# Performance work log

Measured on AMD Instinct MI355X. Metric: run time of the kernel, lower is better.

The kernel has to match this reference:

```python
import jax, jax.numpy as jnp
import numpy as np

B, T, K = 32, 64, 5
VOCAB, DE, DA, DI, H = 32000, 300, 300, 2048, 512


def setup_inputs() -> dict:
    key = jax.random.key(0)
    ks = jax.random.split(key, 8)
    return {
        'top_k_attributes': jax.random.randint(ks[0], (B, K), 0, 1000, dtype=jnp.int32),
        'mean_image_features': jax.random.normal(ks[1], (B, DI), jnp.float32),
        'seq_inputs': jax.random.randint(ks[2], (B, T), 0, VOCAB, dtype=jnp.int32),
        'lengths': jax.random.randint(ks[3], (B,), 1, T + 1, dtype=jnp.int32),
        'word_emb': jax.random.normal(ks[4], (VOCAB, DE), jnp.float32) * 0.02,
        'attr_emb': jax.random.normal(ks[5], (1000, DA), jnp.float32) * 0.02,
        'lstm_kernel': jax.random.normal(ks[6], (DE + DI + DA + H, 4 * H), jnp.float32) * 0.02,
        'lstm_bias': jnp.zeros((4 * H,), jnp.float32),
        'W_logits': jax.random.normal(ks[7], (H, VOCAB), jnp.float32) * 0.02,
        'b_logits': jnp.zeros((VOCAB,), jnp.float32),
    }


def reference(top_k_attributes, mean_image_features, seq_inputs, lengths,
              word_emb, attr_emb, lstm_kernel, lstm_bias, W_logits, b_logits):
    # attribute features: lookup + mean over the K attributes
    attr_feats = attr_emb[top_k_attributes]              # [B,K,DA]
    mean_attr = attr_feats.mean(axis=1)                  # [B,DA]
    feats = jnp.concatenate([mean_image_features, mean_attr], axis=-1)  # [B,DI+DA]

    x = word_emb[seq_inputs]                             # [B,T,DE]
    # per-step cell input = concat(word_emb_t, image+attr features)
    inp = jnp.concatenate([x, jnp.broadcast_to(feats[:, None, :], (B, T, feats.shape[-1]))], axis=-1)

    def step(carry, x_t):
        h, c = carry
        z = jnp.concatenate([x_t, h], axis=-1) @ lstm_kernel + lstm_bias  # [B,4H]
        i, f, g, o = jnp.split(z, 4, axis=-1)
        c = jax.nn.sigmoid(f) * c + jax.nn.sigmoid(i) * jnp.tanh(g)
        h = jax.nn.sigmoid(o) * jnp.tanh(c)
        return (h, c), h

    h0 = jnp.zeros((B, H), inp.dtype)
    (_, _), h_seq = jax.lax.scan(step, (h0, h0), jnp.transpose(inp, (1, 0, 2)))
    h_seq = jnp.transpose(h_seq, (1, 0, 2))              # [B,T,H]

    # dynamic_rnn zeros activations past each sequence length
    mask = (jnp.arange(T)[None, :] < lengths[:, None])[:, :, None]
    h_seq = jnp.where(mask, h_seq, 0.0)

    logits = jnp.einsum('bth,hv->btv', h_seq, W_logits) + b_logits  # [B,T,V]
    return logits, jnp.argmax(logits, axis=-1).astype(jnp.int32)
```

## Files before the change

### kernel.cpp

```cpp
#include <hip/hip_runtime.h>
#include <hip/hip_bf16.h>
#include <math.h>

#define BATCH 32
#define TSEQ  64
#define KATTR 5
#define VOCAB 32000
#define DE    300
#define DA    300
#define DI    2048
#define HDIM  512
#define G4    2048
#define WOFF  (DE + DI + DA)

__global__ void zero_kernel(float* __restrict__ p, int n) {
    int i = blockIdx.x * blockDim.x + threadIdx.x;
    if (i < n) p[i] = 0.f;
}

__global__ void mean_attr_kernel(const int* __restrict__ topk,
                                 const float* __restrict__ attr_emb,
                                 float* __restrict__ mean_attr) {
    int b = blockIdx.x;
    int tid = threadIdx.x;
    if (tid < DA) {
        float s = 0.f;
        #pragma unroll
        for (int q = 0; q < KATTR; ++q) {
            int a = topk[b * KATTR + q];
            s += attr_emb[(size_t)a * DA + tid];
        }
        mean_attr[b * DA + tid] = s / (float)KATTR;
    }
}

__launch_bounds__(256)
__global__ void zf_kernel(const float* __restrict__ img,
                          const float* __restrict__ mean_attr,
                          const float* __restrict__ Wk,
                          const float* __restrict__ bias,
                          float* __restrict__ zf) {
    int b = blockIdx.y;
    int j = blockIdx.x * 256 + threadIdx.x;
    float acc = bias[j];
    const float* wimg = Wk + (size_t)DE * G4 + j;
    const float* irow = img + b * DI;
    #pragma unroll 8
    for (int k = 0; k < DI; ++k) acc += irow[k] * wimg[(size_t)k * G4];
    const float* wattr = Wk + (size_t)(DE + DI) * G4 + j;
    const float* arow = mean_attr + b * DA;
    #pragma unroll 4
    for (int k = 0; k < DA; ++k) acc += arow[k] * wattr[(size_t)k * G4];
    zf[b * G4 + j] = acc;
}

__launch_bounds__(256)
__global__ void whr_kernel(const float* __restrict__ Wk, float* __restrict__ Whr) {
    const int bid = blockIdx.x;
    const int tid = threadIdx.x;
    for (int it = 0; it < 16; ++it) {
        int Q = it * 256 + tid;
        int k = Q >> 3, jj = Q & 7;
        int g = jj >> 1, p = jj & 1;
        Whr[(size_t)bid * 4096 + Q] = Wk[(size_t)(WOFF + k) * G4 + g * HDIM + bid * 2 + p];
    }
}

template<bool GATHER, bool PERROW>
__launch_bounds__(256)
__global__ void gemm_tile(const float* __restrict__ A,
                          const int* __restrict__ gidx,
                          const float* __restrict__ Bm,
                          const float* __restrict__ addv,
                          float* __restrict__ C,
                          int M, int N, int K, int lda) {
    __shared__ __align__(16) float As[16][68];
    __shared__ __align__(16) float Bs[16][68];
    const int tid = threadIdx.x;
    const int n0 = blockIdx.x * 64;
    const int m0 = blockIdx.y * 64;
    const int tx = tid & 15, ty = tid >> 4;
    const int ar  = tid >> 2;
    const int akq = (tid & 3) << 2;
    const int bkr = tid >> 4;
    const int bc  = (tid & 15) << 2;

    size_t arow;
    if (GATHER) arow = (size_t)gidx[m0 + ar] * (size_t)lda;
    else        arow = (size_t)(m0 + ar) * (size_t)lda;

    float a00=0,a01=0,a02=0,a03=0, a10=0,a11=0,a12=0,a13=0;
    float a20=0,a21=0,a22=0,a23=0, a30=0,a31=0,a32=0,a33=0;

    for (int k0 = 0; k0 < K; k0 += 16) {
        int ka = k0 + akq;
        float4 av;
        if (ka + 4 <= K) {
            av = *(const float4*)(A + arow + ka);
        } else {
            av.x = (ka + 0 < K) ? A[arow + ka + 0] : 0.f;
            av.y = (ka + 1 < K) ? A[arow + ka + 1] : 0.f;
            av.z = (ka + 2 < K) ? A[arow + ka + 2] : 0.f;
            av.w = (ka + 3 < K) ? A[arow + ka + 3] : 0.f;
        }
        As[akq + 0][ar] = av.x;
        As[akq + 1][ar] = av.y;
        As[akq + 2][ar] = av.z;
        As[akq + 3][ar] = av.w;

        int kb = k0 + bkr;
        float4 bv;
        if (kb < K) bv = *(const float4*)(Bm + (size_t)kb * N + n0 + bc);
        else { bv.x = bv.y = bv.z = bv.w = 0.f; }
        *(float4*)&Bs[bkr][bc] = bv;

        __syncthreads();
        #pragma unroll
        for (int kk = 0; kk < 16; ++kk) {
            const float4 a4 = *(const float4*)&As[kk][ty << 2];
            const float4 b4 = *(const float4*)&Bs[kk][tx << 2];
            a00 += a4.x * b4.x; a01 += a4.x * b4.y; a02 += a4.x * b4.z; a03 += a4.x * b4.w;
            a10 += a4.y * b4.x; a11 += a4.y * b4.y; a12 += a4.y * b4.z; a13 += a4.y * b4.w;
            a20 += a4.z * b4.x; a21 += a4.z * b4.y; a22 += a4.z * b4.z; a23 += a4.z * b4.w;
            a30 += a4.w * b4.x; a31 += a4.w * b4.y; a32 += a4.w * b4.z; a33 += a4.w * b4.w;
        }
        __syncthreads();
    }

    float accs[4][4] = {{a00,a01,a02,a03},{a10,a11,a12,a13},{a20,a21,a22,a23},{a30,a31,a32,a33}};
    const int n = n0 + (tx << 2);
    #pragma unroll
    for (int i = 0; i < 4; ++i) {
        int m = m0 + (ty << 2) + i;
        const float* av2 = PERROW ? (addv + (size_t)(m >> 6) * N) : addv;
        float4 o;
        o.x = accs[i][0] + av2[n + 0];
        o.y = accs[i][1] + av2[n + 1];
        o.z = accs[i][2] + av2[n + 2];
        o.w = accs[i][3] + av2[n + 3];
        *(float4*)(C + (size_t)m * N + n) = o;
    }
}

__global__ void build_rows(const int* __restrict__ lengths,
                           int* __restrict__ rowlist, int* __restrict__ mact) {
    __shared__ int len[BATCH];
    __shared__ int off[BATCH + 1];
    int tid = threadIdx.x;
    if (tid < BATCH) len[tid] = lengths[tid];
    __syncthreads();
    if (tid == 0) {
        int s = 0;
        for (int b = 0; b < BATCH; ++b) { off[b] = s; s += len[b]; }
        off[BATCH] = s;
        *mact = s;
    }
    __syncthreads();
    int total = off[BATCH];
    for (int i = tid; i < BATCH * TSEQ; i += 256) {
        int b = i >> 6, t = i & 63;
        if (t < len[b]) rowlist[off[b] + t] = i;
    }
    for (int i = tid; i < BATCH * TSEQ; i += 256) {
        if (i >= total) rowlist[i] = 0;
    }
}

__launch_bounds__(256, 1)
__global__ void lstm_step2(const float* __restrict__ z_pre,
                           const float* __restrict__ Whr,
                           const float* __restrict__ hin,
                           float* __restrict__ hout,
                           float* __restrict__ cbuf,
                           float* __restrict__ h_seq,
                           const int* __restrict__ lengths,
                           int t) {
    __shared__ __align__(16) float hsT[HDIM][36];
    __shared__ __align__(16) float wsm[HDIM][12];
    __shared__ __align__(16) float zp[16 * 260];
    __shared__ float zfull[BATCH][8];
    const int bid = blockIdx.x;
    const int tid = threadIdx.x;

    float zp4[4] = {0, 0, 0, 0};
    int glen = 0, gb = 0, gkk = 0;
    float c_old = 0.f;
    if (tid < 64) {
        gb = tid & 31;
        int kp = tid >> 5;
        gkk = bid * 2 + kp;
        glen = lengths[gb];
        const float* zr = z_pre + ((size_t)(gb * TSEQ + t)) * G4 + gkk;
        zp4[0] = zr[0 * HDIM];
        zp4[1] = zr[1 * HDIM];
        zp4[2] = zr[2 * HDIM];
        zp4[3] = zr[3 * HDIM];
        c_old = cbuf[gkk * BATCH + gb];
    }

    #pragma unroll
    for (int it = 0; it < 16; ++it) {
        int Q = it * 256 + tid;
        int k = Q >> 3, bq = Q & 7;
        float4 v = *(const float4*)(hin + (size_t)Q * 4);
        *(float4*)&hsT[k][bq * 4] = v;
    }
    const float* wsrc = Whr + (size_t)bid * 4096;
    #pragma unroll
    for (int it = 0; it < 4; ++it) {
        int Q = it * 256 + tid;
        int k = Q >> 1, jjq = Q & 1;
        float4 v = *(const float4*)(wsrc + (size_t)Q * 4);
        *(float4*)&wsm[k][jjq * 4] = v;
    }
    __syncthreads();

    {
        const int kseg = tid >> 4;
        const int tile = tid & 15;
        const int b0 = (tile >> 1) << 2;
        const int j0 = (tile & 1) << 2;
        const int kb = kseg << 5;
        float a00=0,a01=0,a02=0,a03=0, a10=0,a11=0,a12=0,a13=0;
        float a20=0,a21=0,a22=0,a23=0, a30=0,a31=0,a32=0,a33=0;
        #pragma unroll 8
        for (int kk = 0; kk < 32; ++kk) {
            const int k = kb + kk;
            const float4 h4 = *(const float4*)&hsT[k][b0];
            const float4 w4 = *(const float4*)&wsm[k][j0];
            a00 += h4.x * w4.x; a01 += h4.x * w4.y; a02 += h4.x * w4.z; a03 += h4.x * w4.w;
            a10 += h4.y * w4.x; a11 += h4.y * w4.y; a12 += h4.y * w4.z; a13 += h4.y * w4.w;
            a20 += h4.z * w4.x; a21 += h4.z * w4.y; a22 += h4.z * w4.z; a23 += h4.z * w4.w;
            a30 += h4.w * w4.x; a31 += h4.w * w4.y; a32 += h4.w * w4.z; a33 += h4.w * w4.w;
        }
        float* zpr = &zp[kseg * 260 + tile * 16];
        *(float4*)(zpr + 0)  = make_float4(a00, a01, a02, a03);
        *(float4*)(zpr + 4)  = make_float4(a10, a11, a12, a13);
        *(float4*)(zpr + 8)  = make_float4(a20, a21, a22, a23);
        *(float4*)(zpr + 12) = make_float4(a30, a31, a32, a33);
    }
    __syncthreads();

    {
        const int b = tid & 31, jj = tid >> 5;
        const int tile2 = ((b >> 2) << 1) + (jj >> 2);
        const int e = ((b & 3) << 2) + (jj & 3);
        float s = 0.f;
        #pragma unroll
        for (int ks = 0; ks < 16; ++ks) s += zp[ks * 260 + tile2 * 16 + e];
        zfull[b][jj] = s;
    }
    __syncthreads();

    if (tid < 64) {
        const int kp = tid >> 5;
        float zi = zfull[gb][0 * 2 + kp] + zp4[0];
        float zF = zfull[gb][1 * 2 + kp] + zp4[1];
        float zg = zfull[gb][2 * 2 + kp] + zp4[2];
        float zo = zfull[gb][3 * 2 + kp] + zp4[3];
        float si = 1.f / (1.f + expf(-zi));
        float sf = 1.f / (1.f + expf(-zF));
        float so = 1.f / (1.f + expf(-zo));
        float c_new = sf * c_old + si * tanhf(zg);
        float h_new = so * tanhf(c_new);
        cbuf[gkk * BATCH + gb] = c_new;
        hout[gkk * BATCH + gb] = h_new;
        h_seq[((size_t)(gb * TSEQ + t)) * HDIM + gkk] = (t < glen) ? h_new : 0.f;
    }
}

__launch_bounds__(256)
__global__ void fill_masked(const int* __restrict__ lengths,
                            const float* __restrict__ blog,
                            float* __restrict__ logits) {
    int row = blockIdx.x;
    int b = row >> 6, t = row & 63;
    if (t < lengths[b]) return;
    float* p = logits + (size_t)row * VOCAB;
    for (int v = threadIdx.x * 4; v < VOCAB; v += 256 * 4) {
        float4 o;
        o.x = blog[v + 0]; o.y = blog[v + 1]; o.z = blog[v + 2]; o.w = blog[v + 3];
        *(float4*)(p + v) = o;
    }
}

__launch_bounds__(256)
__global__ void gemm_logits128(const float* __restrict__ A,
                               const int* __restrict__ rowlist,
                               const int* __restrict__ mactp,
                               const float* __restrict__ Bm,
                               const float* __restrict__ blog,
                               float* __restrict__ C) {
    const int Mact = *mactp;
    const int chunk = gridDim.x >> 3;
    const int L = (blockIdx.x & 7) * chunk + (blockIdx.x >> 3);
    const int m0 = (L & 15) * 128;
    const int n0 = (L >> 4) * 128;
    if (m0 >= Mact) return;

    __shared__ __align__(16) float As[16][132];
    __shared__ __align__(16) float Bs[16][132];
    const int tid = threadIdx.x;
    const int tx = tid & 15, ty = tid >> 4;

    const int am  = tid >> 2;
    const int akq = (tid & 3) << 2;
    const size_t arow0 = (size_t)rowlist[m0 + am]      * HDIM;
    const size_t arow1 = (size_t)rowlist[m0 + 64 + am] * HDIM;
    const int bk = tid >> 5;
    const int bc = (tid & 31) << 2;

    float c00[4][4] = {}, c01[4][4] = {}, c10[4][4] = {}, c11[4][4] = {};

    for (int k0 = 0; k0 < HDIM; k0 += 16) {
        const float4 av0 = *(const float4*)(A + arow0 + k0 + akq);
        const float4 av1 = *(const float4*)(A + arow1 + k0 + akq);
        As[akq + 0][am] = av0.x;
        As[akq + 1][am] = av0.y;
        As[akq + 2][am] = av0.z;
        As[akq + 3][am] = av0.w;
        As[akq + 0][64 + am] = av1.x;
        As[akq + 1][64 + am] = av1.y;
        As[akq + 2][64 + am] = av1.z;
        As[akq + 3][64 + am] = av1.w;
        const float4 bv0 = *(const float4*)(Bm + (size_t)(k0 + bk)     * VOCAB + n0 + bc);
        const float4 bv1 = *(const float4*)(Bm + (size_t)(k0 + 8 + bk) * VOCAB + n0 + bc);
        *(float4*)&Bs[bk][bc]     = bv0;
        *(float4*)&Bs[bk + 8][bc] = bv1;
        __syncthreads();
        #pragma unroll
        for (int kk = 0; kk < 16; ++kk) {
            const float4 aL = *(const float4*)&As[kk][ty << 2];
            const float4 aH = *(const float4*)&As[kk][64 + (ty << 2)];
            const float4 bL = *(const float4*)&Bs[kk][tx << 2];
            const float4 bH = *(const float4*)&Bs[kk][64 + (tx << 2)];
            const float a_[8] = {aL.x, aL.y, aL.z, aL.w, aH.x, aH.y, aH.z, aH.w};
            const float b_[8] = {bL.x, bL.y, bL.z, bL.w, bH.x, bH.y, bH.z, bH.w};
            #pragma unroll
            for (int i = 0; i < 4; ++i) {
                #pragma unroll
                for (int j = 0; j < 4; ++j) {
                    c00[i][j] += a_[i]     * b_[j];
                    c01[i][j] += a_[i]     * b_[4 + j];
                    c10[i][j] += a_[4 + i] * b_[j];
                    c11[i][j] += a_[4 + i] * b_[4 + j];
                }
            }
        }
        __syncthreads();
    }

    const int nL = n0 + (tx << 2);
    const int nH = nL + 64;
    const float4 gL = *(const float4*)(blog + nL);
    const float4 gH = *(const float4*)(blog + nH);
    const float gLa[4] = {gL.x, gL.y, gL.z, gL.w};
    const float gHa[4] = {gH.x, gH.y, gH.z, gH.w};
    #pragma unroll
    for (int i = 0; i < 4; ++i) {
        const int mL = m0 + (ty << 2) + i;
        if (mL < Mact) {
            const size_t rm = (size_t)rowlist[mL] * VOCAB;
            float4 oL, oH;
            oL.x = c00[i][0] + gLa[0]; oL.y = c00[i][1] + gLa[1];
            oL.z = c00[i][2] + gLa[2]; oL.w = c00[i][3] + gLa[3];
            oH.x = c01[i][0] + gHa[0]; oH.y = c01[i][1] + gHa[1];
            oH.z = c01[i][2] + gHa[2]; oH.w = c01[i][3] + gHa[3];
            *(float4*)(C + rm + nL) = oL;
            *(float4*)(C + rm + nH) = oH;
        }
        const int mH = mL + 64;
        if (mH < Mact) {
            const size_t rm = (size_t)rowlist[mH] * VOCAB;
            float4 oL, oH;
            oL.x = c10[i][0] + gLa[0]; oL.y = c10[i][1] + gLa[1];
            oL.z = c10[i][2] + gLa[2]; oL.w = c10[i][3] + gLa[3];
            oH.x = c11[i][0] + gHa[0]; oH.y = c11[i][1] + gHa[1];
            oH.z = c11[i][2] + gHa[2]; oH.w = c11[i][3] + gHa[3];
            *(float4*)(C + rm + nL) = oL;
            *(float4*)(C + rm + nH) = oH;
        }
    }
}

__launch_bounds__(256)
__global__ void argmax_kernel(const float* __restrict__ logits, float* __restrict__ outa) {
    const int row = blockIdx.x;
    const int tid = threadIdx.x;
    const float* p = logits + (size_t)row * VOCAB;
    float bv = -INFINITY; int bi = VOCAB;
    for (int v = tid; v < VOCAB; v += 256) {
        float x = p[v];
        if (x > bv) { bv = x; bi = v; }
    }
    __shared__ float sv[256];
    __shared__ int   si[256];
    sv[tid] = bv; si[tid] = bi;
    __syncthreads();
    for (int s = 128; s > 0; s >>= 1) {
        if (tid < s) {
            if (sv[tid + s] > sv[tid] || (sv[tid + s] == sv[tid] && si[tid + s] < si[tid])) {
                sv[tid] = sv[tid + s]; si[tid] = si[tid + s];
            }
        }
        __syncthreads();
    }
    if (tid == 0) outa[row] = (float)si[0];
}

extern "C" void kernel_launch(void* const* d_in, const int* in_sizes, int n_in,
                              void* d_out, int out_size, void* d_ws, size_t ws_size,
                              hipStream_t stream) {
    const int*   topk     = (const int*)d_in[0];
    const float* img      = (const float*)d_in[1];
    const int*   seq      = (const int*)d_in[2];
    const int*   lengths  = (const int*)d_in[3];
    const float* word_emb = (const float*)d_in[4];
    const float* attr_emb = (const float*)d_in[5];
    const float* Wk       = (const float*)d_in[6];
    const float* bias     = (const float*)d_in[7];
    const float* Wlog     = (const float*)d_in[8];
    const float* blog     = (const float*)d_in[9];

    float* out_logits = (float*)d_out;
    float* out_argmax = out_logits + (size_t)BATCH * TSEQ * VOCAB;

    float* ws        = (float*)d_ws;
    float* mean_attr = ws;
    float* zf        = mean_attr + BATCH * DA;
    float* cbuf      = zf + BATCH * G4;
    float* hb0       = cbuf + HDIM * BATCH;
    float* hb1       = hb0 + HDIM * BATCH;
    float* h_seq     = hb1 + HDIM * BATCH;
    float* Whr       = h_seq + (size_t)BATCH * TSEQ * HDIM;
    int*   rowlist   = (int*)(Whr + (size_t)256 * 4096);
    int*   mact      = rowlist + BATCH * TSEQ;
    float* z_pre     = out_logits;

    zero_kernel<<<dim3((2 * HDIM * BATCH + 255) / 256), 256, 0, stream>>>(cbuf, 2 * HDIM * BATCH);

    build_rows<<<1, 256, 0, stream>>>(lengths, rowlist, mact);

    whr_kernel<<<dim3(256), 256, 0, stream>>>(Wk, Whr);

    mean_attr_kernel<<<dim3(BATCH), 320, 0, stream>>>(topk, attr_emb, mean_attr);

    zf_kernel<<<dim3(G4 / 256, BATCH), 256, 0, stream>>>(img, mean_attr, Wk, bias, zf);

    gemm_tile<true, true><<<dim3(G4 / 64, (BATCH * TSEQ) / 64), 256, 0, stream>>>(
        word_emb, seq, Wk, zf, z_pre, BATCH * TSEQ, G4, DE, DE);

    float* hin = hb0;
    float* hout = hb1;
    for (int t = 0; t < TSEQ; ++t) {
        lstm_step2<<<dim3(256), 256, 0, stream>>>(z_pre, Whr, hin, hout, cbuf, h_seq, lengths, t);
        float* tmp = hin; hin = hout; hout = tmp;
    }

    fill_masked<<<dim3(BATCH * TSEQ), 256, 0, stream>>>(lengths, blog, out_logits);

    gemm_logits128<<<dim3((VOCAB / 128) * ((BATCH * TSEQ) / 128)), 256, 0, stream>>>(
        h_seq, rowlist, mact, Wlog, blog, out_logits);

    argmax_kernel<<<dim3(BATCH * TSEQ), 256, 0, stream>>>(out_logits, out_argmax);
}
```

Measured before the change: 1.408 ms.

## Fuse per-step LSTM launches into one persistent cooperative kernel with grid sync

Replaces the 64 per-timestep lstm_step2 launches with a single cooperative lstm_scan kernel that loops over time and uses grid.sync() between steps. Each block's slice of the recurrent weights is loaded into shared memory once rather than every step, and the cell state now stays in registers instead of a global buffer. This removes launch overhead and repeated weight reloads, but relies on all 256 blocks being co-resident and on a grid-wide barrier after every step.

```diff
diff --git a/kernel.cpp b/kernel.cpp
--- a/kernel.cpp
+++ b/kernel.cpp
@@ -1,6 +1,9 @@
 #include <hip/hip_runtime.h>
 #include <hip/hip_bf16.h>
+#include <hip/hip_cooperative_groups.h>
 #include <math.h>
+
+namespace cg = cooperative_groups;
 
 #define BATCH 32
 #define TSEQ  64
@@ -167,44 +170,20 @@
 }
 
 __launch_bounds__(256, 1)
-__global__ void lstm_step2(const float* __restrict__ z_pre,
-                           const float* __restrict__ Whr,
-                           const float* __restrict__ hin,
-                           float* __restrict__ hout,
-                           float* __restrict__ cbuf,
-                           float* __restrict__ h_seq,
-                           const int* __restrict__ lengths,
-                           int t) {
+__global__ void lstm_scan(const float* __restrict__ z_pre,
+                          const float* __restrict__ Whr,
+                          float* __restrict__ hb0,
+                          float* __restrict__ hb1,
+                          float* __restrict__ h_seq,
+                          const int* __restrict__ lengths) {
     __shared__ __align__(16) float hsT[HDIM][36];
     __shared__ __align__(16) float wsm[HDIM][12];
     __shared__ __align__(16) float zp[16 * 260];
     __shared__ float zfull[BATCH][8];
     const int bid = blockIdx.x;
     const int tid = threadIdx.x;
-
-    float zp4[4] = {0, 0, 0, 0};
-    int glen = 0, gb = 0, gkk = 0;
-    float c_old = 0.f;
-    if (tid < 64) {
-        gb = tid & 31;
-        int kp = tid >> 5;
-        gkk = bid * 2 + kp;
-        glen = lengths[gb];
-        const float* zr = z_pre + ((size_t)(gb * TSEQ + t)) * G4 + gkk;
-        zp4[0] = zr[0 * HDIM];
-        zp4[1] = zr[1 * HDIM];
-        zp4[2] = zr[2 * HDIM];
-        zp4[3] = zr[3 * HDIM];
-        c_old = cbuf[gkk * BATCH + gb];
-    }
-
-    #pragma unroll
-    for (int it = 0; it < 16; ++it) {
-        int Q = it * 256 + tid;
-        int k = Q >> 3, bq = Q & 7;
-        float4 v = *(const float4*)(hin + (size_t)Q * 4);
-        *(float4*)&hsT[k][bq * 4] = v;
-    }
+    cg::grid_group grid = cg::this_grid();
+
     const float* wsrc = Whr + (size_t)bid * 4096;
     #pragma unroll
     for (int it = 0; it < 4; ++it) {
@@ -213,59 +192,93 @@
         float4 v = *(const float4*)(wsrc + (size_t)Q * 4);
         *(float4*)&wsm[k][jjq * 4] = v;
     }
-    __syncthreads();
-
-    {
-        const int kseg = tid >> 4;
-        const int tile = tid & 15;
-        const int b0 = (tile >> 1) << 2;
-        const int j0 = (tile & 1) << 2;
-        const int kb = kseg << 5;
-        float a00=0,a01=0,a02=0,a03=0, a10=0,a11=0,a12=0,a13=0;
-        float a20=0,a21=0,a22=0,a23=0, a30=0,a31=0,a32=0,a33=0;
-        #pragma unroll 8
-        for (int kk = 0; kk < 32; ++kk) {
-            const int k = kb + kk;
-            const float4 h4 = *(const float4*)&hsT[k][b0];
-            const float4 w4 = *(const float4*)&wsm[k][j0];
-            a00 += h4.x * w4.x; a01 += h4.x * w4.y; a02 += h4.x * w4.z; a03 += h4.x * w4.w;
-            a10 += h4.y * w4.x; a11 += h4.y * w4.y; a12 += h4.y * w4.z; a13 += h4.y * w4.w;
-            a20 += h4.z * w4.x; a21 += h4.z * w4.y; a22 += h4.z * w4.z; a23 += h4.z * w4.w;
-            a30 += h4.w * w4.x; a31 += h4.w * w4.y; a32 += h4.w * w4.z; a33 += h4.w * w4.w;
-        }
-        float* zpr = &zp[kseg * 260 + tile * 16];
-        *(float4*)(zpr + 0)  = make_float4(a00, a01, a02, a03);
-        *(float4*)(zpr + 4)  = make_float4(a10, a11, a12, a13);
-        *(float4*)(zpr + 8)  = make_float4(a20, a21, a22, a23);
-        *(float4*)(zpr + 12) = make_float4(a30, a31, a32, a33);
-    }
-    __syncthreads();
-
-    {
-        const int b = tid & 31, jj = tid >> 5;
-        const int tile2 = ((b >> 2) << 1) + (jj >> 2);
-        const int e = ((b & 3) << 2) + (jj & 3);
-        float s = 0.f;
+
+    int glen = 0, gb = 0, gkk = 0;
+    float c_reg = 0.f;
+    const float* zr = nullptr;
+    if (tid < 64) {
+        gb = tid & 31;
+        int kp = tid >> 5;
+        gkk = bid * 2 + kp;
+        glen = lengths[gb];
+        zr = z_pre + ((size_t)(gb * TSEQ)) * G4 + gkk;
+    }
+
+    const int kseg = tid >> 4;
+    const int tile = tid & 15;
+    const int b0 = (tile >> 1) << 2;
+    const int j0 = (tile & 1) << 2;
+    const int kb = kseg << 5;
+    const int rb = tid & 31, rjj = tid >> 5;
+    const int tile2 = ((rb >> 2) << 1) + (rjj >> 2);
+    const int e = ((rb & 3) << 2) + (rjj & 3);
+
+    for (int t = 0; t < TSEQ; ++t) {
+        const float* hin  = (t & 1) ? hb1 : hb0;
+        float*       hout = (t & 1) ? hb0 : hb1;
+
+        float zp4[4] = {0, 0, 0, 0};
+        if (tid < 64) {
+            const float* z = zr + (size_t)t * G4;
+            zp4[0] = z[0 * HDIM];
+            zp4[1] = z[1 * HDIM];
+            zp4[2] = z[2 * HDIM];
+            zp4[3] = z[3 * HDIM];
+        }
+
         #pragma unroll
-        for (int ks = 0; ks < 16; ++ks) s += zp[ks * 260 + tile2 * 16 + e];
-        zfull[b][jj] = s;
-    }
-    __syncthreads();
-
-    if (tid < 64) {
-        const int kp = tid >> 5;
-        float zi = zfull[gb][0 * 2 + kp] + zp4[0];
-        float zF = zfull[gb][1 * 2 + kp] + zp4[1];
-        float zg = zfull[gb][2 * 2 + kp] + zp4[2];
-        float zo = zfull[gb][3 * 2 + kp] + zp4[3];
-        float si = 1.f / (1.f + expf(-zi));
-        float sf = 1.f / (1.f + expf(-zF));
-        float so = 1.f / (1.f + expf(-zo));
-        float c_new = sf * c_old + si * tanhf(zg);
-        float h_new = so * tanhf(c_new);
-        cbuf[gkk * BATCH + gb] = c_new;
-        hout[gkk * BATCH + gb] = h_new;
-        h_seq[((size_t)(gb * TSEQ + t)) * HDIM + gkk] = (t < glen) ? h_new : 0.f;
+        for (int it = 0; it < 16; ++it) {
+            int Q = it * 256 + tid;
+            int k = Q >> 3, bq = Q & 7;
+            float4 v = *(const float4*)(hin + (size_t)Q * 4);
+            *(float4*)&hsT[k][bq * 4] = v;
+        }
+        __syncthreads();
+
+        {
+            float a00=0,a01=0,a02=0,a03=0, a10=0,a11=0,a12=0,a13=0;
+            float a20=0,a21=0,a22=0,a23=0, a30=0,a31=0,a32=0,a33=0;
+            #pragma unroll 8
+            for (int kk = 0; kk < 32; ++kk) {
+                const int k = kb + kk;
+                const float4 h4 = *(const float4*)&hsT[k][b0];
+                const float4 w4 = *(const float4*)&wsm[k][j0];
+                a00 += h4.x * w4.x; a01 += h4.x * w4.y; a02 += h4.x * w4.z; a03 += h4.x * w4.w;
+                a10 += h4.y * w4.x; a11 += h4.y * w4.y; a12 += h4.y * w4.z; a13 += h4.y * w4.w;
+                a20 += h4.z * w4.x; a21 += h4.z * w4.y; a22 += h4.z * w4.z; a23 += h4.z * w4.w;
+                a30 += h4.w * w4.x; a31 += h4.w * w4.y; a32 += h4.w * w4.z; a33 += h4.w * w4.w;
+            }
+            float* zpr = &zp[kseg * 260 + tile * 16];
+            *(float4*)(zpr + 0)  = make_float4(a00, a01, a02, a03);
+            *(float4*)(zpr + 4)  = make_float4(a10, a11, a12, a13);
+            *(float4*)(zpr + 8)  = make_float4(a20, a21, a22, a23);
+            *(float4*)(zpr + 12) = make_float4(a30, a31, a32, a33);
+        }
+        __syncthreads();
+
+        {
+            float s = 0.f;
+            #pragma unroll
+            for (int ks = 0; ks < 16; ++ks) s += zp[ks * 260 + tile2 * 16 + e];
+            zfull[rb][rjj] = s;
+        }
+        __syncthreads();
+
+        if (tid < 64) {
+            float zi = zfull[gb][0 * 2 + (tid >> 5)] + zp4[0];
+            float zF = zfull[gb][1 * 2 + (tid >> 5)] + zp4[1];
+            float zg = zfull[gb][2 * 2 + (tid >> 5)] + zp4[2];
+            float zo = zfull[gb][3 * 2 + (tid >> 5)] + zp4[3];
+            float si = 1.f / (1.f + expf(-zi));
+            float sf = 1.f / (1.f + expf(-zF));
+            float so = 1.f / (1.f + expf(-zo));
+            float c_new = sf * c_reg + si * tanhf(zg);
+            float h_new = so * tanhf(c_new);
+            c_reg = c_new;
+            hout[gkk * BATCH + gb] = h_new;
+            h_seq[((size_t)(gb * TSEQ + t)) * HDIM + gkk] = (t < glen) ? h_new : 0.f;
+        }
+        grid.sync();
     }
 }
 
@@ -437,7 +450,7 @@
     int*   mact      = rowlist + BATCH * TSEQ;
     float* z_pre     = out_logits;
 
-    zero_kernel<<<dim3((2 * HDIM * BATCH + 255) / 256), 256, 0, stream>>>(cbuf, 2 * HDIM * BATCH);
+    zero_kernel<<<dim3((2 * HDIM * BATCH + 255) / 256), 256, 0, stream>>>(hb0, 2 * HDIM * BATCH);
 
     build_rows<<<1, 256, 0, stream>>>(lengths, rowlist, mact);
 
@@ -450,11 +463,11 @@
     gemm_tile<true, true><<<dim3(G4 / 64, (BATCH * TSEQ) / 64), 256, 0, stream>>>(
         word_emb, seq, Wk, zf, z_pre, BATCH * TSEQ, G4, DE, DE);
 
-    float* hin = hb0;
-    float* hout = hb1;
-    for (int t = 0; t < TSEQ; ++t) {
-        lstm_step2<<<dim3(256), 256, 0, stream>>>(z_pre, Whr, hin, hout, cbuf, h_seq, lengths, t);
-        float* tmp = hin; hin = hout; hout = tmp;
+    {
+        void* kargs[] = {(void*)&z_pre, (void*)&Whr, (void*)&hb0, (void*)&hb1,
+                         (void*)&h_seq, (void*)&lengths};
+        hipLaunchCooperativeKernel((const void*)lstm_scan, dim3(256), dim3(256),
+                                   kargs, 0, stream);
     }
 
     fill_masked<<<dim3(BATCH * TSEQ), 256, 0, stream>>>(lengths, blog, out_logits);
```

Result: slower. 3.181 ms (+126.0%).

## Fuse argmax into logits GEMM epilogue via packed atomicMax

Applied to the files above, without the earlier changes.

Computes per-row argmax inside the logits GEMM epilogue. Each row's value and index are packed into an order-preserving 64-bit key, reduced across 16 lanes with shuffles, and merged globally with atomicMax. A tiny finalize kernel then writes indices, using the bias argmax for masked rows. This removes a full re-read of the 262MB logits tensor by the separate argmax kernel, at the cost of extra epilogue work and atomics. Masked rows hold only the bias, so their argmax is the argmax of b_logits.

```diff
diff --git a/kernel.cpp b/kernel.cpp
--- a/kernel.cpp
+++ b/kernel.cpp
@@ -16,6 +16,15 @@
 __global__ void zero_kernel(float* __restrict__ p, int n) {
     int i = blockIdx.x * blockDim.x + threadIdx.x;
     if (i < n) p[i] = 0.f;
+}
+
+__device__ __forceinline__ unsigned int fkey(float f) {
+    unsigned int u = __float_as_uint(f);
+    return (u & 0x80000000u) ? ~u : (u | 0x80000000u);
+}
+__device__ __forceinline__ void amax_upd(unsigned int& bk, int& bi, float v, int idx) {
+    unsigned int k = fkey(v);
+    if (k > bk || (k == bk && idx < bi)) { bk = k; bi = idx; }
 }
 
 __global__ void mean_attr_kernel(const int* __restrict__ topk,
@@ -290,7 +299,8 @@
                                const int* __restrict__ mactp,
                                const float* __restrict__ Bm,
                                const float* __restrict__ blog,
-                               float* __restrict__ C) {
+                               float* __restrict__ C,
+                               unsigned long long* __restrict__ packed) {
     const int Mact = *mactp;
     const int chunk = gridDim.x >> 3;
     const int L = (blockIdx.x & 7) * chunk + (blockIdx.x >> 3);
@@ -360,7 +370,8 @@
     for (int i = 0; i < 4; ++i) {
         const int mL = m0 + (ty << 2) + i;
         if (mL < Mact) {
-            const size_t rm = (size_t)rowlist[mL] * VOCAB;
+            const int rid = rowlist[mL];
+            const size_t rm = (size_t)rid * VOCAB;
             float4 oL, oH;
             oL.x = c00[i][0] + gLa[0]; oL.y = c00[i][1] + gLa[1];
             oL.z = c00[i][2] + gLa[2]; oL.w = c00[i][3] + gLa[3];
@@ -368,10 +379,26 @@
             oH.z = c01[i][2] + gHa[2]; oH.w = c01[i][3] + gHa[3];
             *(float4*)(C + rm + nL) = oL;
             *(float4*)(C + rm + nH) = oH;
+            unsigned int bkk = 0u; int bii = 0x7FFFFFFF;
+            amax_upd(bkk, bii, oL.x, nL + 0); amax_upd(bkk, bii, oL.y, nL + 1);
+            amax_upd(bkk, bii, oL.z, nL + 2); amax_upd(bkk, bii, oL.w, nL + 3);
+            amax_upd(bkk, bii, oH.x, nH + 0); amax_upd(bkk, bii, oH.y, nH + 1);
+            amax_upd(bkk, bii, oH.z, nH + 2); amax_upd(bkk, bii, oH.w, nH + 3);
+            unsigned long long pv = ((unsigned long long)bkk << 32) | (unsigned int)(~bii);
+            #pragma unroll
+            for (int off = 8; off > 0; off >>= 1) {
+                unsigned int hi = (unsigned int)(pv >> 32), lo = (unsigned int)pv;
+                unsigned int ohi = __shfl_xor(hi, off, 16);
+                unsigned int olo = __shfl_xor(lo, off, 16);
+                unsigned long long ov = ((unsigned long long)ohi << 32) | olo;
+                if (ov > pv) pv = ov;
+            }
+            if (tx == 0) atomicMax(&packed[rid], pv);
         }
         const int mH = mL + 64;
         if (mH < Mact) {
-            const size_t rm = (size_t)rowlist[mH] * VOCAB;
+            const int rid = rowlist[mH];
+            const size_t rm = (size_t)rid * VOCAB;
             float4 oL, oH;
             oL.x = c10[i][0] + gLa[0]; oL.y = c10[i][1] + gLa[1];
             oL.z = c10[i][2] + gLa[2]; oL.w = c10[i][3] + gLa[3];
@@ -379,33 +406,51 @@
             oH.z = c11[i][2] + gHa[2]; oH.w = c11[i][3] + gHa[3];
             *(float4*)(C + rm + nL) = oL;
             *(float4*)(C + rm + nH) = oH;
+            unsigned int bkk = 0u; int bii = 0x7FFFFFFF;
+            amax_upd(bkk, bii, oL.x, nL + 0); amax_upd(bkk, bii, oL.y, nL + 1);
+            amax_upd(bkk, bii, oL.z, nL + 2); amax_upd(bkk, bii, oL.w, nL + 3);
+            amax_upd(bkk, bii, oH.x, nH + 0); amax_upd(bkk, bii, oH.y, nH + 1);
+            amax_upd(bkk, bii, oH.z, nH + 2); amax_upd(bkk, bii, oH.w, nH + 3);
+            unsigned long long pv = ((unsigned long long)bkk << 32) | (unsigned int)(~bii);
+            #pragma unroll
+            for (int off = 8; off > 0; off >>= 1) {
+                unsigned int hi = (unsigned int)(pv >> 32), lo = (unsigned int)pv;
+                unsigned int ohi = __shfl_xor(hi, off, 16);
+                unsigned int olo = __shfl_xor(lo, off, 16);
+                unsigned long long ov = ((unsigned long long)ohi << 32) | olo;
+                if (ov > pv) pv = ov;
+            }
+            if (tx == 0) atomicMax(&packed[rid], pv);
         }
     }
 }
 
 __launch_bounds__(256)
-__global__ void argmax_kernel(const float* __restrict__ logits, float* __restrict__ outa) {
-    const int row = blockIdx.x;
+__global__ void finalize_argmax(const unsigned long long* __restrict__ packed,
+                                const float* __restrict__ blog,
+                                const int* __restrict__ lengths,
+                                float* __restrict__ outa) {
+    __shared__ unsigned long long red[256];
+    __shared__ int slen[BATCH];
     const int tid = threadIdx.x;
-    const float* p = logits + (size_t)row * VOCAB;
-    float bv = -INFINITY; int bi = VOCAB;
+    unsigned int bk = 0u; int bi = 0x7FFFFFFF;
     for (int v = tid; v < VOCAB; v += 256) {
-        float x = p[v];
-        if (x > bv) { bv = x; bi = v; }
-    }
-    __shared__ float sv[256];
-    __shared__ int   si[256];
-    sv[tid] = bv; si[tid] = bi;
+        amax_upd(bk, bi, blog[v], v);
+    }
+    red[tid] = ((unsigned long long)bk << 32) | (unsigned int)(~bi);
+    if (tid < BATCH) slen[tid] = lengths[tid];
     __syncthreads();
     for (int s = 128; s > 0; s >>= 1) {
-        if (tid < s) {
-            if (sv[tid + s] > sv[tid] || (sv[tid + s] == sv[tid] && si[tid + s] < si[tid])) {
-                sv[tid] = sv[tid + s]; si[tid] = si[tid + s];
-            }
-        }
+        if (tid < s) { if (red[tid + s] > red[tid]) red[tid] = red[tid + s]; }
         __syncthreads();
     }
-    if (tid == 0) outa[row] = (float)si[0];
+    const int bias_idx = (int)(~(unsigned int)(red[0] & 0xFFFFFFFFull));
+    for (int row = tid; row < BATCH * TSEQ; row += 256) {
+        int b = row >> 6, t = row & 63;
+        int idx = (t < slen[b]) ? (int)(~(unsigned int)(packed[row] & 0xFFFFFFFFull))
+                                : bias_idx;
+        outa[row] = (float)idx;
+    }
 }
 
 extern "C" void kernel_launch(void* const* d_in, const int* in_sizes, int n_in,
@@ -435,9 +480,11 @@
     float* Whr       = h_seq + (size_t)BATCH * TSEQ * HDIM;
     int*   rowlist   = (int*)(Whr + (size_t)256 * 4096);
     int*   mact      = rowlist + BATCH * TSEQ;
+    unsigned long long* packed = (unsigned long long*)(mact + 2);
     float* z_pre     = out_logits;
 
     zero_kernel<<<dim3((2 * HDIM * BATCH + 255) / 256), 256, 0, stream>>>(cbuf, 2 * HDIM * BATCH);
+    zero_kernel<<<dim3(16), 256, 0, stream>>>((float*)packed, 4096);
 
     build_rows<<<1, 256, 0, stream>>>(lengths, rowlist, mact);
 
@@ -460,7 +507,7 @@
     fill_masked<<<dim3(BATCH * TSEQ), 256, 0, stream>>>(lengths, blog, out_logits);
 
     gemm_logits128<<<dim3((VOCAB / 128) * ((BATCH * TSEQ) / 128)), 256, 0, stream>>>(
-        h_seq, rowlist, mact, Wlog, blog, out_logits);
-
-    argmax_kernel<<<dim3(BATCH * TSEQ), 256, 0, stream>>>(out_logits, out_argmax);
-}
+        h_seq, rowlist, mact, Wlog, blog, out_logits, packed);
+
+    finalize_argmax<<<dim3(1), 256, 0, stream>>>(packed, blog, lengths, out_argmax);
+}
```

Result: no change. 1.382 ms (-1.9%).
